# Kernel optimization log

Hardware: AMD Instinct MI355X
Metric: run time of the kernel (lower is better)

## Reference

```python
import jax, jax.numpy as jnp
import numpy as np

H = 4                      # num_heads hard-coded in SDHGNN
NAMES = ["self", "cross", "self", "cross"]
POOL_SIZES = [2, 2, 2, 2]
MIN_NGHS = 128             # minium_nghs
EPS = 1e-3                 # InstanceNorm1d eps


def _pw(x, W, b):
    # pointwise Conv1d(kernel=1): [B, Cin, N] -> [B, Cout, N]
    return jnp.einsum('oi,bin->bon', W, x) + b[None, :, None]


def _instnorm(x):
    # InstanceNorm1d (no affine): normalize over N per (B, C)
    m = jnp.mean(x, axis=2, keepdims=True)
    v = jnp.mean((x - m) ** 2, axis=2, keepdims=True)
    return (x - m) * jax.lax.rsqrt(v + EPS)


def _attn_prop(x, src, p):
    # SharedAttentionalPropagation (sharing_attention=False):
    # MultiHeadedAttention + concat + MLP residual update.
    Wq, bq, Wk, bk, Wv, bv, Wm, bm, W1, b1, W2, b2 = p
    B, D, N = x.shape
    dh = D // H
    q = _pw(x, Wq, bq).reshape(B, dh, H, N)
    k = _pw(src, Wk, bk).reshape(B, dh, H, -1)
    v = _pw(src, Wv, bv).reshape(B, dh, H, -1)
    scores = jnp.einsum('bdhn,bdhm->bhnm', q, k) * (dh ** -0.5)
    prob = jax.nn.softmax(scores, axis=-1)                     # [B,H,N,M]
    msg = jnp.einsum('bhnm,bdhm->bdhn', prob, v).reshape(B, D, N)
    msg = _pw(msg, Wm, bm)
    y = jnp.concatenate([x, msg], axis=1)                      # [B,2D,N]
    h = jax.nn.relu(_instnorm(_pw(y, W1, b1)))
    return x + _pw(h, W2, b2), prob


def _gather(x, idx):
    # x: [B,D,N], idx: [B,K] -> [B,D,K]
    return jnp.take_along_axis(
        x, jnp.broadcast_to(idx[:, None, :], (x.shape[0], x.shape[1], idx.shape[1])), axis=2)


def _pool(prob, idx, pool_size):
    # pooling_by_prob (4-D prob branch): mean over heads, sum over queries,
    # top-k by importance, sorted indices, gather global indexes.
    K = idx.shape[1]
    p = prob.mean(axis=1).sum(axis=1)                          # [B,K]
    k = min(max(K // pool_size, MIN_NGHS), K)
    _, top = jax.lax.top_k(p, k)
    top = jnp.sort(top, axis=1)
    return jnp.take_along_axis(idx, top, axis=1)


def setup_inputs() -> dict:
    key = jax.random.key(0)
    B, D, N, L = 2, 128, 2048, 4
    ks = jax.random.split(key, 16)
    s = lambda fan: 1.0 / np.sqrt(fan)
    inp = {
        'x0': jax.random.normal(ks[0], (B, D, N), jnp.float32),
        'x1': jax.random.normal(ks[1], (B, D, N), jnp.float32),
        'Wq': jax.random.normal(ks[2], (L, D, D), jnp.float32) * s(D),
        'bq': jax.random.normal(ks[3], (L, D), jnp.float32) * 0.01,
        'Wk': jax.random.normal(ks[4], (L, D, D), jnp.float32) * s(D),
        'bk': jax.random.normal(ks[5], (L, D), jnp.float32) * 0.01,
        'Wv': jax.random.normal(ks[6], (L, D, D), jnp.float32) * s(D),
        'bv': jax.random.normal(ks[7], (L, D), jnp.float32) * 0.01,
        'Wm': jax.random.normal(ks[8], (L, D, D), jnp.float32) * s(D),
        'bm': jax.random.normal(ks[9], (L, D), jnp.float32) * 0.01,
        'W1': jax.random.normal(ks[10], (L, 2 * D, 2 * D), jnp.float32) * s(2 * D),
        'b1': jax.random.normal(ks[11], (L, 2 * D), jnp.float32) * 0.01,
        'W2': jax.random.normal(ks[12], (L, D, 2 * D), jnp.float32) * s(2 * D),
        'b2': jnp.zeros((L, D), jnp.float32),  # nn.init.constant_(mlp[-1].bias, 0)
    }
    return inp


def reference(x0, x1, Wq, bq, Wk, bk, Wv, bv, Wm, bm, W1, b1, W2, b2):
    B, D, N = x0.shape
    idx0 = jnp.broadcast_to(jnp.arange(N, dtype=jnp.int32)[None], (B, N))
    idx1 = idx0
    for l, (name, ps) in enumerate(zip(NAMES, POOL_SIZES)):
        p = (Wq[l], bq[l], Wk[l], bk[l], Wv[l], bv[l],
             Wm[l], bm[l], W1[l], b1[l], W2[l], b2[l])
        if name == 'self':
            s0, s1 = _gather(x0, idx0), _gather(x1, idx1)
        else:
            s0, s1 = _gather(x1, idx1), _gather(x0, idx0)
        x0, prob0 = _attn_prop(x0, s0, p)
        x1, prob1 = _attn_prop(x1, s1, p)
        if name == 'self':
            idx0 = _pool(prob0, idx0, ps)
            idx1 = _pool(prob1, idx1, ps)
        else:
            idx1 = _pool(prob0, idx1, ps)
            idx0 = _pool(prob1, idx0, ps)
    return jnp.stack([x0, x1], axis=0)   # [2, B, D, N]
```

## Files before the change

kernel.cpp:

```cpp
#include <hip/hip_runtime.h>
#include <cstdint>
#include <cstddef>


#define NB 2
#define ND 128
#define NH 4
#define NN 2048
#define ND2 256
#define DN (ND*NN)
#define BDN (NB*DN)
#define QK_SCALE 0.2550348623f
#define IN_EPS 1e-3f

typedef unsigned short u16;
typedef __attribute__((ext_vector_type(8))) short short8;
typedef __attribute__((ext_vector_type(4))) float f32x4;

__device__ __forceinline__ u16 f2bf(float f) {
    unsigned u = __float_as_uint(f);
    return (u16)((u + 0x7fffu + ((u >> 16) & 1u)) >> 16);
}
__device__ __forceinline__ float bf2f(u16 h) {
    return __uint_as_float(((unsigned)h) << 16);
}
__device__ __forceinline__ float fexp2(float x) {
#if __has_builtin(__builtin_amdgcn_exp2f)
    return __builtin_amdgcn_exp2f(x);
#else
    return exp2f(x);
#endif
}
__device__ __forceinline__ unsigned cvtpk_bf16(float a, float b) {
    unsigned r;
    asm("v_cvt_pk_bf16_f32 %0, %1, %2" : "=v"(r) : "v"(a), "v"(b));
    return r;
}
#define ROR16F(x, N) __int_as_float(__builtin_amdgcn_update_dpp( \
    0, __float_as_int(x), 0x120 + (N), 0xF, 0xF, true))

__global__ __launch_bounds__(256) void init_kernel(
    const float* __restrict__ x0in, const float* __restrict__ x1in,
    float* __restrict__ out, int* __restrict__ idx0, int* __restrict__ idx1)
{
    int tid = blockIdx.x * 256 + threadIdx.x;
    const float4* a = (const float4*)x0in;
    const float4* b = (const float4*)x1in;
    float4* o = (float4*)out;
    o[tid] = a[tid];
    o[BDN/4 + tid] = b[tid];
    if (tid < NB*NN) {
        int v = tid & (NN-1);
        idx0[tid] = v;
        idx1[tid] = v;
    }
}

__global__ __launch_bounds__(256) void wrepack2_kernel(
    const float* __restrict__ Wq, const float* __restrict__ Wk,
    const float* __restrict__ Wv, const float* __restrict__ Wm,
    const float* __restrict__ W1, const float* __restrict__ W2,
    const float* __restrict__ bq, const float* __restrict__ bk,
    const float* __restrict__ bv, const float* __restrict__ bm,
    const float* __restrict__ b1,
    u16* __restrict__ whi, u16* __restrict__ wlo,
    float* __restrict__ bqp, float* __restrict__ bkp, float* __restrict__ bvp,
    float* __restrict__ b1p)
{
    int e = blockIdx.x * 256 + threadIdx.x;
    if (e < 655360) {
        int l = e / 163840, r = e - l*163840;
        float v;
        if (r < 49152) {
            int m = r >> 14;
            int rr = r & 16383;
            int o = rr >> 7, c = rr & 127;
            int so = (o & 31)*4 + (o >> 5);
            const float* W = (m == 0) ? Wq : ((m == 1) ? Wk : Wv);
            v = W[l*16384 + so*128 + c];
        } else if (r < 65536) {
            int rr = r - 49152;
            int o = rr >> 7, c = rr & 127;
            int sc = (c & 31)*4 + (c >> 5);
            v = Wm[l*16384 + o*128 + sc];
        } else if (r < 131072) {
            int rr = r - 65536;
            int c = rr & 255;
            if (c < 128) {
                v = W1[l*65536 + rr];
            } else {
                int o = rr >> 8, cc = c - 128;
                int sc = (cc & 31)*4 + (cc >> 5);
                const float* w1row = &W1[l*65536 + o*256 + 128];
                const float* wmcol = &Wm[l*16384 + sc];
                float acc = 0.f;
                #pragma unroll 4
                for (int k = 0; k < 128; ++k)
                    acc = fmaf(w1row[k], wmcol[k*128], acc);
                v = acc;
            }
        }
        else                   v = W2[l*32768 + r - 131072];
        u16 hb = f2bf(v);
        whi[e] = hb;
        wlo[e] = f2bf(v - bf2f(hb));
    } else if (e < 656896) {
        int eb = e - 655360;
        int l = eb / 384, rr = eb % 384;
        int which = rr >> 7, o = rr & 127;
        int so = (o & 31)*4 + (o >> 5);
        float v = (which == 0 ? bq : (which == 1 ? bk : bv))[l*128 + so];
        (which == 0 ? bqp : (which == 1 ? bkp : bvp))[l*128 + o] = v;
    } else if (e < 657920) {
        int idx = e - 656896;
        int l = idx >> 8, o = idx & 255;
        const float* w1row = &W1[l*65536 + o*256 + 128];
        const float* bmv = &bm[l*128];
        float acc = b1[l*256 + o];
        #pragma unroll 4
        for (int k = 0; k < 128; ++k)
            acc = fmaf(w1row[k], bmv[k], acc);
        b1p[l*256 + o] = acc;
    }
}

__global__ __launch_bounds__(256) void repack_xh_kernel(
    const float* __restrict__ in, u16* __restrict__ ohi, u16* __restrict__ olo)
{
    __shared__ float tile[32][68];
    int z = blockIdx.y >> 2, cg = blockIdx.y & 3;
    int n0 = blockIdx.x * 64;
    int t = threadIdx.x;
    {
        int i = t >> 3, nc = (t & 7) * 8;
        const float* src = &in[((size_t)z*128 + cg*32 + i)*NN + n0 + nc];
        float4 a = *(const float4*)src;
        float4 b = *(const float4*)(src + 4);
        tile[i][nc+0]=a.x; tile[i][nc+1]=a.y; tile[i][nc+2]=a.z; tile[i][nc+3]=a.w;
        tile[i][nc+4]=b.x; tile[i][nc+5]=b.y; tile[i][nc+6]=b.z; tile[i][nc+7]=b.w;
    }
    __syncthreads();
    int n = t >> 2, c8 = (t & 3) * 8;
    short8 hi, lo;
    #pragma unroll
    for (int j = 0; j < 8; ++j) {
        float v = tile[c8 + j][n];
        u16 h = f2bf(v);
        hi[j] = (short)h;
        lo[j] = (short)f2bf(v - bf2f(h));
    }
    size_t ob = ((size_t)z*NN + n0 + n)*128 + cg*32 + c8;
    *(short8*)&ohi[ob] = hi;
    *(short8*)&olo[ob] = lo;
}

__device__ __forceinline__ void gcore(
    u16* As0, u16* As1, u16* Bs0, u16* Bs1,
    const u16* __restrict__ Whi, const u16* __restrict__ Wlo, int o0, int Cin,
    const u16* __restrict__ B1hi, const u16* __restrict__ B1lo, int s1,
    const u16* __restrict__ B2hi, const u16* __restrict__ B2lo, int s2, int split,
    size_t brow, int n0, const int* __restrict__ idxp, int t, f32x4 acc[2][2])
{
    const int lane = t & 63, w = t >> 6;
    const int l15 = lane & 15, quad = lane >> 4;
    const int wr = (w & 1)*32, wc = (w >> 1)*32;
    const int ao = t >> 2, ak = (t & 3)*8;
    int grow = n0 + ao;
    if (idxp) grow = idxp[grow];

    short8 rA0, rA1, rB0, rB1;
    {
        size_t wa = (size_t)(o0 + ao)*Cin + ak;
        rA0 = *(const short8*)&Whi[wa];
        rA1 = *(const short8*)&Wlo[wa];
        int c = ak;
        const u16 *ph, *pl; size_t off;
        if (c < split) { ph = B1hi; pl = B1lo; off = (brow + grow)*s1 + c; }
        else { ph = B2hi; pl = B2lo; off = (brow + grow)*s2 + (c - split); }
        rB0 = *(const short8*)&ph[off];
        rB1 = *(const short8*)&pl[off];
    }
    for (int kc = 0; kc < Cin; kc += 32) {
        __syncthreads();
        *(short8*)&As0[ao*40 + ak] = rA0;
        *(short8*)&As1[ao*40 + ak] = rA1;
        *(short8*)&Bs0[ao*40 + ak] = rB0;
        *(short8*)&Bs1[ao*40 + ak] = rB1;
        if (kc + 32 < Cin) {
            size_t wa = (size_t)(o0 + ao)*Cin + kc + 32 + ak;
            rA0 = *(const short8*)&Whi[wa];
            rA1 = *(const short8*)&Wlo[wa];
            int c = kc + 32 + ak;
            const u16 *ph, *pl; size_t off;
            if (c < split) { ph = B1hi; pl = B1lo; off = (brow + grow)*s1 + c; }
            else { ph = B2hi; pl = B2lo; off = (brow + grow)*s2 + (c - split); }
            rB0 = *(const short8*)&ph[off];
            rB1 = *(const short8*)&pl[off];
        }
        __syncthreads();
        short8 Ah[2], Al[2], Bh[2], Bl[2];
        #pragma unroll
        for (int a = 0; a < 2; ++a) {
            Ah[a] = *(const short8*)&As0[(wr + a*16 + l15)*40 + quad*8];
            Al[a] = *(const short8*)&As1[(wr + a*16 + l15)*40 + quad*8];
        }
        #pragma unroll
        for (int c = 0; c < 2; ++c) {
            Bh[c] = *(const short8*)&Bs0[(wc + c*16 + l15)*40 + quad*8];
            Bl[c] = *(const short8*)&Bs1[(wc + c*16 + l15)*40 + quad*8];
        }
        #pragma unroll
        for (int a = 0; a < 2; ++a)
            #pragma unroll
            for (int c = 0; c < 2; ++c) {
                acc[a][c] = __builtin_amdgcn_mfma_f32_16x16x32_bf16(Ah[a], Bl[c], acc[a][c], 0,0,0);
                acc[a][c] = __builtin_amdgcn_mfma_f32_16x16x32_bf16(Al[a], Bh[c], acc[a][c], 0,0,0);
                acc[a][c] = __builtin_amdgcn_mfma_f32_16x16x32_bf16(Ah[a], Bh[c], acc[a][c], 0,0,0);
            }
    }
    __syncthreads();
}

__device__ __forceinline__ void gcore_w2(
    u16* As0, u16* As1, u16* Bs0, u16* Bs1,
    const u16* __restrict__ Whi, const u16* __restrict__ Wlo, int o0,
    const float* __restrict__ zft, const float* __restrict__ meanL,
    const float* __restrict__ ivL,
    size_t brow, int n0, int t, f32x4 acc[2][2])
{
    const int Cin = 256;
    const int lane = t & 63, w = t >> 6;
    const int l15 = lane & 15, quad = lane >> 4;
    const int wr = (w & 1)*32, wc = (w >> 1)*32;
    const int ao = t >> 2, ak = (t & 3)*8;
    const float* brows = &zft[(brow + n0 + ao)*256];

    short8 rA0, rA1, rBh, rBl;
    {
        size_t wa = (size_t)(o0 + ao)*Cin + ak;
        rA0 = *(const short8*)&Whi[wa];
        rA1 = *(const short8*)&Wlo[wa];
        float4 f0 = *(const float4*)&brows[ak];
        float4 f1 = *(const float4*)&brows[ak + 4];
        float f[8] = {f0.x,f0.y,f0.z,f0.w,f1.x,f1.y,f1.z,f1.w};
        #pragma unroll
        for (int j = 0; j < 8; ++j) {
            float v = (f[j] - meanL[ak + j]) * ivL[ak + j];
            v = v > 0.f ? v : 0.f;
            u16 hb = f2bf(v);
            rBh[j] = (short)hb;
            rBl[j] = (short)f2bf(v - bf2f(hb));
        }
    }
    for (int kc = 0; kc < Cin; kc += 32) {
        __syncthreads();
        *(short8*)&As0[ao*40 + ak] = rA0;
        *(short8*)&As1[ao*40 + ak] = rA1;
        *(short8*)&Bs0[ao*40 + ak] = rBh;
        *(short8*)&Bs1[ao*40 + ak] = rBl;
        float4 f0n, f1n;
        const bool more = (kc + 32 < Cin);
        if (more) {
            size_t wa = (size_t)(o0 + ao)*Cin + kc + 32 + ak;
            rA0 = *(const short8*)&Whi[wa];
            rA1 = *(const short8*)&Wlo[wa];
            f0n = *(const float4*)&brows[kc + 32 + ak];
            f1n = *(const float4*)&brows[kc + 32 + ak + 4];
        }
        __syncthreads();
        short8 Ah[2], Al[2], Bh[2], Bl[2];
        #pragma unroll
        for (int a = 0; a < 2; ++a) {
            Ah[a] = *(const short8*)&As0[(wr + a*16 + l15)*40 + quad*8];
            Al[a] = *(const short8*)&As1[(wr + a*16 + l15)*40 + quad*8];
        }
        #pragma unroll
        for (int c = 0; c < 2; ++c) {
            Bh[c] = *(const short8*)&Bs0[(wc + c*16 + l15)*40 + quad*8];
            Bl[c] = *(const short8*)&Bs1[(wc + c*16 + l15)*40 + quad*8];
        }
        #pragma unroll
        for (int a = 0; a < 2; ++a)
            #pragma unroll
            for (int c = 0; c < 2; ++c) {
                acc[a][c] = __builtin_amdgcn_mfma_f32_16x16x32_bf16(Ah[a], Bl[c], acc[a][c], 0,0,0);
                acc[a][c] = __builtin_amdgcn_mfma_f32_16x16x32_bf16(Al[a], Bh[c], acc[a][c], 0,0,0);
                acc[a][c] = __builtin_amdgcn_mfma_f32_16x16x32_bf16(Ah[a], Bh[c], acc[a][c], 0,0,0);
            }
        if (more) {
            float f[8] = {f0n.x,f0n.y,f0n.z,f0n.w,f1n.x,f1n.y,f1n.z,f1n.w};
            #pragma unroll
            for (int j = 0; j < 8; ++j) {
                int cc = kc + 32 + ak + j;
                float v = (f[j] - meanL[cc]) * ivL[cc];
                v = v > 0.f ? v : 0.f;
                u16 hb = f2bf(v);
                rBh[j] = (short)hb;
                rBl[j] = (short)f2bf(v - bf2f(hb));
            }
        }
    }
    __syncthreads();
}

__global__ __launch_bounds__(256) void qkv_kernel(
    const u16* __restrict__ Whi, const u16* __restrict__ Wlo,
    const float* __restrict__ bqp, const float* __restrict__ bkp,
    const float* __restrict__ bvp,
    const u16* __restrict__ xphi, const u16* __restrict__ xplo,
    const int* __restrict__ idx0, const int* __restrict__ idx1,
    int cross, int M,
    u16* __restrict__ qthi, u16* __restrict__ qtlo,
    u16* __restrict__ kthi, u16* __restrict__ ktlo,
    u16* __restrict__ vthi, float* __restrict__ p,
    float* __restrict__ gsum, float* __restrict__ gsq)
{
    __shared__ u16 gsm[10240];
    u16* As0 = gsm;  u16* As1 = gsm + 2560;
    u16* Bs0 = gsm + 5120; u16* Bs1 = gsm + 7680;
    float* tb = (float*)gsm;

    const int z = blockIdx.z;
    const int bx = blockIdx.x;
    const int t = threadIdx.x;
    const int lane = t & 63, w = t >> 6;
    const int l15 = lane & 15, quad = lane >> 4;
    const int wr = (w & 1)*32, wc = (w >> 1)*32;

    int role, o0, n0, nCols;
    const u16 *Wbh, *Wbl;
    const float* bias;
    if (bx < 64) {
        role = 0; o0 = (bx & 1)*64; n0 = (bx >> 1)*64; nCols = NN;
        Wbh = Whi; Wbl = Wlo; bias = bqp;
        if (t < 32) p[(size_t)z*NN + bx*32 + t] = 0.f;
        if (bx == 0) { gsum[z*256 + t] = 0.f; gsq[z*256 + t] = 0.f; }
    } else {
        int e = bx - 64;
        int kt = M >> 6;
        int ct = e % kt, rt = e / kt;
        n0 = ct*64; nCols = M;
        if (rt < 2) { role = 1; o0 = rt*64; Wbh = Whi+16384; Wbl = Wlo+16384; bias = bkp; }
        else        { role = 2; o0 = (rt-2)*64; Wbh = Whi+32768; Wbl = Wlo+32768; bias = bvp; }
    }
    size_t brow = (size_t)z * NN;
    const int* idxp = nullptr;
    if (role != 0) {
        int ss = cross ? 1 - (z >> 1) : (z >> 1);
        brow = (size_t)(ss*2 + (z & 1)) * NN;
        idxp = (ss ? idx1 : idx0) + (z & 1)*NN;
    }

    f32x4 acc[2][2];
    #pragma unroll
    for (int a = 0; a < 2; ++a)
        #pragma unroll
        for (int c = 0; c < 2; ++c) acc[a][c] = (f32x4){0.f,0.f,0.f,0.f};

    gcore(As0, As1, Bs0, Bs1, Wbh, Wbl, o0, 128,
          xphi, xplo, 128, xphi, xplo, 128, 128, brow, n0, idxp, t, acc);

    if (role == 2) {
        #pragma unroll
        for (int a = 0; a < 2; ++a)
            #pragma unroll
            for (int c = 0; c < 2; ++c)
                #pragma unroll
                for (int r = 0; r < 4; ++r) {
                    int row = o0 + wr + a*16 + quad*4 + r;
                    int m = n0 + wc + c*16 + l15;
                    float v = acc[a][c][r] + bias[row];
                    vthi[((size_t)(z*4 + (row>>5))*32 + (row&31))*(size_t)M + m] = f2bf(v);
                }
    } else {
        float scale = role ? 1.f : QK_SCALE;
        #pragma unroll
        for (int a = 0; a < 2; ++a)
            #pragma unroll
            for (int c = 0; c < 2; ++c)
                #pragma unroll
                for (int r = 0; r < 4; ++r) {
                    int rl = wr + a*16 + quad*4 + r;
                    tb[rl*66 + wc + c*16 + l15] = acc[a][c][r] + bias[o0 + rl];
                }
        __syncthreads();
        u16* ohi = role ? kthi : qthi;
        u16* olo = role ? ktlo : qtlo;
        int n = t >> 2, rb = (t & 3)*16;
        #pragma unroll
        for (int g = 0; g < 2; ++g) {
            short8 hi, lo;
            #pragma unroll
            for (int j = 0; j < 8; ++j) {
                float v = tb[(rb + g*8 + j)*66 + n] * scale;
                u16 hb = f2bf(v);
                hi[j] = (short)hb;
                lo[j] = (short)f2bf(v - bf2f(hb));
            }
            int rowg = o0 + rb + g*8;
            size_t ob = ((size_t)(z*4 + (rowg >> 5))*nCols + n0 + n)*32 + (rowg & 31);
            *(short8*)&ohi[ob] = hi;
            *(short8*)&olo[ob] = lo;
        }
    }
}

__global__ __launch_bounds__(512, 4) void attn4_kernel(
    const u16* __restrict__ qthi, const u16* __restrict__ qtlo,
    const u16* __restrict__ kthi, const u16* __restrict__ ktlo,
    const u16* __restrict__ vthi, int M,
    u16* __restrict__ msghi, u16* __restrict__ msglo, float* __restrict__ p)
{
    __shared__ float pcolA[2048], pcolB[2048];
    __shared__ float obuf[96*66];
    __shared__ float redm[4][64], redl[4][64];
    __shared__ float rowM[64], rowIV[64];

    const int t = threadIdx.x;
    const int lane = t & 63, wave = t >> 6;
    const int l15 = lane & 15, quad = lane >> 4;
    const int qp = wave & 1, mh = wave >> 1;
    const int h = blockIdx.y, z = blockIdx.z;
    const int zh = z*4 + h;
    const int n0 = blockIdx.x * 64;

    for (int i = t; i < M; i += 512) { pcolA[i] = 0.f; pcolB[i] = 0.f; }

    short8 qBh[2], qBl[2];
    #pragma unroll
    for (int qt = 0; qt < 2; ++qt) {
        size_t qb = ((size_t)zh*NN + n0 + qp*32 + qt*16 + l15)*32 + quad*8;
        qBh[qt] = *(const short8*)&qthi[qb];
        qBl[qt] = *(const short8*)&qtlo[qb];
    }

    const int nch = M >> 7;
    const size_t kb0 = ((size_t)zh*M + mh*32 + l15)*32 + quad*8;
    const u16* kbh = kthi + kb0;
    const u16* kbl = ktlo + kb0;
    const u16* vb = vthi + ((size_t)zh*32 + l15)*M + mh*32 + quad*8;

    float rm[2] = {-1e30f, -1e30f}, rl[2] = {0.f, 0.f};

    for (int ch = 0; ch < nch; ++ch) {
        const int co = ch*128*32;
        #pragma unroll
        for (int mt = 0; mt < 2; ++mt) {
            short8 kh = *(const short8*)&kbh[co + mt*512];
            short8 kl = *(const short8*)&kbl[co + mt*512];
            __builtin_amdgcn_s_setprio(1);
            f32x4 av[2];
            #pragma unroll
            for (int qt = 0; qt < 2; ++qt) {
                f32x4 a = {0.f,0.f,0.f,0.f};
                a = __builtin_amdgcn_mfma_f32_16x16x32_bf16(kh, qBl[qt], a, 0,0,0);
                a = __builtin_amdgcn_mfma_f32_16x16x32_bf16(kl, qBh[qt], a, 0,0,0);
                a = __builtin_amdgcn_mfma_f32_16x16x32_bf16(kh, qBh[qt], a, 0,0,0);
                av[qt] = a;
            }
            __builtin_amdgcn_s_setprio(0);
            #pragma unroll
            for (int qt = 0; qt < 2; ++qt) {
                f32x4 a = av[qt];
                float bm = fmaxf(fmaxf(a[0],a[1]), fmaxf(a[2],a[3]));
                float bs = fexp2(a[0]-bm)+fexp2(a[1]-bm)+fexp2(a[2]-bm)+fexp2(a[3]-bm);
                if (bm > rm[qt]) { rl[qt] = rl[qt]*fexp2(rm[qt]-bm) + bs; rm[qt] = bm; }
                else rl[qt] += bs*fexp2(bm - rm[qt]);
            }
        }
    }

    #pragma unroll
    for (int qt = 0; qt < 2; ++qt) {
        #pragma unroll
        for (int off = 16; off <= 32; off <<= 1) {
            float om = __shfl_xor(rm[qt], off);
            float ol = __shfl_xor(rl[qt], off);
            float nm = fmaxf(rm[qt], om);
            rl[qt] = rl[qt]*fexp2(rm[qt]-nm) + ol*fexp2(om-nm);
            rm[qt] = nm;
        }
        if (quad == 0) {
            redm[mh][qp*32 + qt*16 + l15] = rm[qt];
            redl[mh][qp*32 + qt*16 + l15] = rl[qt];
        }
    }
    __syncthreads();
    if (t < 64) {
        float m = redm[0][t], l = redl[0][t];
        #pragma unroll
        for (int w2 = 1; w2 < 4; ++w2) {
            float om = redm[w2][t];
            float nm = fmaxf(m, om);
            l = l*fexp2(m - nm) + redl[w2][t]*fexp2(om - nm);
            m = nm;
        }
        rowM[t] = m;
        rowIV[t] = 1.f / l;
    }
    __syncthreads();
    float myRM[2], myRIV[2];
    #pragma unroll
    for (int qt = 0; qt < 2; ++qt) {
        myRM[qt]  = rowM[qp*32 + qt*16 + l15];
        myRIV[qt] = rowIV[qp*32 + qt*16 + l15];
    }

    f32x4 oa[2][2];
    #pragma unroll
    for (int qt = 0; qt < 2; ++qt)
        #pragma unroll
        for (int dt = 0; dt < 2; ++dt) oa[qt][dt] = (f32x4){0.f,0.f,0.f,0.f};

    const int aA = (l15 + 32*(quad & 1))*4;
    const int aB = aA + 64;
    const bool mtsel = (quad >= 2);
    float* pcolQ = qp ? pcolB : pcolA;

    for (int ch = 0; ch < nch; ++ch) {
        const int m0 = ch << 7;
        const int co = ch*128*32;

        float pr[2][2][4];
        #pragma unroll
        for (int mt = 0; mt < 2; ++mt) {
            short8 kh = *(const short8*)&kbh[co + mt*512];
            short8 kl = *(const short8*)&kbl[co + mt*512];
            __builtin_amdgcn_s_setprio(1);
            f32x4 av[2];
            #pragma unroll
            for (int qt = 0; qt < 2; ++qt) {
                f32x4 a = {0.f,0.f,0.f,0.f};
                a = __builtin_amdgcn_mfma_f32_16x16x32_bf16(kh, qBl[qt], a, 0,0,0);
                a = __builtin_amdgcn_mfma_f32_16x16x32_bf16(kl, qBh[qt], a, 0,0,0);
                a = __builtin_amdgcn_mfma_f32_16x16x32_bf16(kh, qBh[qt], a, 0,0,0);
                av[qt] = a;
            }
            __builtin_amdgcn_s_setprio(0);
            #pragma unroll
            for (int qt = 0; qt < 2; ++qt)
                #pragma unroll
                for (int r = 0; r < 4; ++r)
                    pr[qt][mt][r] = fexp2(av[qt][r] - myRM[qt]);
        }

        #pragma unroll
        for (int mt = 0; mt < 2; ++mt)
            #pragma unroll
            for (int r = 0; r < 4; ++r) {
                float ps = pr[0][mt][r]*myRIV[0] + pr[1][mt][r]*myRIV[1];
                ps += ROR16F(ps, 8);
                ps += ROR16F(ps, 4);
                ps += ROR16F(ps, 2);
                ps += ROR16F(ps, 1);
                if (l15 == 0)
                    pcolQ[m0 + mh*32 + mt*16 + quad*4 + r] = ps;
            }

        short8 vA[2];
        #pragma unroll
        for (int dt = 0; dt < 2; ++dt)
            vA[dt] = *(const short8*)&vb[(size_t)dt*16*M + m0];

        #pragma unroll
        for (int qt = 0; qt < 2; ++qt) {
            unsigned pk00 = cvtpk_bf16(pr[qt][0][0], pr[qt][0][1]);
            unsigned pk01 = cvtpk_bf16(pr[qt][0][2], pr[qt][0][3]);
            unsigned pk10 = cvtpk_bf16(pr[qt][1][0], pr[qt][1][1]);
            unsigned pk11 = cvtpk_bf16(pr[qt][1][2], pr[qt][1][3]);
            unsigned a0 = (unsigned)__builtin_amdgcn_ds_bpermute(aA, (int)pk00);
            unsigned a1 = (unsigned)__builtin_amdgcn_ds_bpermute(aA, (int)pk01);
            unsigned a2 = (unsigned)__builtin_amdgcn_ds_bpermute(aA, (int)pk10);
            unsigned a3 = (unsigned)__builtin_amdgcn_ds_bpermute(aA, (int)pk11);
            unsigned b0 = (unsigned)__builtin_amdgcn_ds_bpermute(aB, (int)pk00);
            unsigned b1 = (unsigned)__builtin_amdgcn_ds_bpermute(aB, (int)pk01);
            unsigned b2 = (unsigned)__builtin_amdgcn_ds_bpermute(aB, (int)pk10);
            unsigned b3 = (unsigned)__builtin_amdgcn_ds_bpermute(aB, (int)pk11);
            union { unsigned u[4]; short8 s; } fb;
            fb.u[0] = mtsel ? a2 : a0;
            fb.u[1] = mtsel ? a3 : a1;
            fb.u[2] = mtsel ? b2 : b0;
            fb.u[3] = mtsel ? b3 : b1;
            __builtin_amdgcn_s_setprio(1);
            #pragma unroll
            for (int dt = 0; dt < 2; ++dt)
                oa[qt][dt] = __builtin_amdgcn_mfma_f32_16x16x32_bf16(vA[dt], fb.s, oa[qt][dt], 0,0,0);
            __builtin_amdgcn_s_setprio(0);
        }
    }

    if (mh > 0) {
        #pragma unroll
        for (int qt = 0; qt < 2; ++qt)
            #pragma unroll
            for (int dt = 0; dt < 2; ++dt)
                #pragma unroll
                for (int r = 0; r < 4; ++r) {
                    int q = qp*32 + qt*16 + l15;
                    int d = dt*16 + quad*4 + r;
                    obuf[((mh-1)*32 + d)*66 + q] = oa[qt][dt][r];
                }
    }
    __syncthreads();
    if (mh == 0) {
        #pragma unroll
        for (int qt = 0; qt < 2; ++qt)
            #pragma unroll
            for (int dt = 0; dt < 2; ++dt)
                #pragma unroll
                for (int r = 0; r < 4; ++r) {
                    int q = qp*32 + qt*16 + l15;
                    int d = dt*16 + quad*4 + r;
                    float v = oa[qt][dt][r];
                    #pragma unroll
                    for (int w2 = 0; w2 < 3; ++w2)
                        v += obuf[(w2*32 + d)*66 + q];
                    obuf[d*66 + q] = v * myRIV[qt];
                }
    }
    __syncthreads();
    {
        int tt = t & 255;
        int n = tt >> 2, i8 = (tt & 3)*8;
        short8 o8;
        if (t < 256) {
            #pragma unroll
            for (int j = 0; j < 8; ++j) o8[j] = (short)f2bf(obuf[(i8+j)*66 + n]);
            *(short8*)&msghi[((size_t)z*NN + n0 + n)*128 + h*32 + i8] = o8;
        } else {
            #pragma unroll
            for (int j = 0; j < 8; ++j) {
                float v = obuf[(i8+j)*66 + n];
                u16 hb = f2bf(v);
                o8[j] = (short)f2bf(v - bf2f(hb));
            }
            *(short8*)&msglo[((size_t)z*NN + n0 + n)*128 + h*32 + i8] = o8;
        }
    }
    for (int i = t; i < M; i += 512)
        atomicAdd(&p[(size_t)z*NN + i], (pcolA[i] + pcolB[i])*0.25f);
}

__global__ __launch_bounds__(256) void w1_kernel(
    const u16* __restrict__ W1h, const u16* __restrict__ W1l,
    const float* __restrict__ b1,
    const u16* __restrict__ xphi, const u16* __restrict__ xplo,
    const u16* __restrict__ m2hi, const u16* __restrict__ m2lo,
    float* __restrict__ zft, float* __restrict__ gsum, float* __restrict__ gsq)
{
    __shared__ u16 gsm[10240];
    u16* As0 = gsm;  u16* As1 = gsm + 2560;
    u16* Bs0 = gsm + 5120; u16* Bs1 = gsm + 7680;
    float* tb = (float*)gsm;

    const int z = blockIdx.z, o0 = blockIdx.y*64, n0 = blockIdx.x*64;
    const int t = threadIdx.x;
    const int lane = t & 63, w = t >> 6;
    const int l15 = lane & 15, quad = lane >> 4;
    const int wr = (w & 1)*32, wc = (w >> 1)*32;

    f32x4 acc[2][2];
    #pragma unroll
    for (int a = 0; a < 2; ++a)
        #pragma unroll
        for (int c = 0; c < 2; ++c) acc[a][c] = (f32x4){0.f,0.f,0.f,0.f};
    gcore(As0, As1, Bs0, Bs1, W1h, W1l, o0, 256,
          xphi, xplo, 128, m2hi, m2lo, 128, 128,
          (size_t)z*NN, n0, nullptr, t, acc);

    float ssum[2][4], ssq[2][4];
    #pragma unroll
    for (int a = 0; a < 2; ++a)
        #pragma unroll
        for (int r = 0; r < 4; ++r) { ssum[a][r] = 0.f; ssq[a][r] = 0.f; }
    #pragma unroll
    for (int a = 0; a < 2; ++a)
        #pragma unroll
        for (int c = 0; c < 2; ++c)
            #pragma unroll
            for (int r = 0; r < 4; ++r) {
                int rl = wr + a*16 + quad*4 + r;
                int cl = wc + c*16 + l15;
                float v = acc[a][c][r] + b1[o0 + rl];
                tb[rl*66 + cl] = v;
                ssum[a][r] += v;
                ssq[a][r] = fmaf(v, v, ssq[a][r]);
            }
    #pragma unroll
    for (int a = 0; a < 2; ++a)
        #pragma unroll
        for (int r = 0; r < 4; ++r) {
            float s = ssum[a][r], q2 = ssq[a][r];
            #pragma unroll
            for (int o = 1; o < 16; o <<= 1) {
                s  += __shfl_xor(s, o);
                q2 += __shfl_xor(q2, o);
            }
            if (l15 == 0) {
                int row = o0 + wr + a*16 + quad*4 + r;
                atomicAdd(&gsum[z*256 + row], s);
                atomicAdd(&gsq[z*256 + row], q2);
            }
        }
    __syncthreads();
    int n = t >> 2, rb = (t & 3)*16;
    #pragma unroll
    for (int g = 0; g < 2; ++g) {
        float4 v0, v1;
        v0.x = tb[(rb + g*8 + 0)*66 + n];
        v0.y = tb[(rb + g*8 + 1)*66 + n];
        v0.z = tb[(rb + g*8 + 2)*66 + n];
        v0.w = tb[(rb + g*8 + 3)*66 + n];
        v1.x = tb[(rb + g*8 + 4)*66 + n];
        v1.y = tb[(rb + g*8 + 5)*66 + n];
        v1.z = tb[(rb + g*8 + 6)*66 + n];
        v1.w = tb[(rb + g*8 + 7)*66 + n];
        float* dst = &zft[((size_t)z*NN + n0 + n)*256 + o0 + rb + g*8];
        *(float4*)dst = v0;
        *(float4*)(dst + 4) = v1;
    }
}

__global__ __launch_bounds__(256) void w2_kernel(
    const u16* __restrict__ W2h, const u16* __restrict__ W2l,
    const float* __restrict__ b2,
    const float* __restrict__ zft, const float* __restrict__ gsum,
    const float* __restrict__ gsq,
    float* __restrict__ out, u16* __restrict__ xphi, u16* __restrict__ xplo,
    int writeplanes)
{
    __shared__ u16 gsm[10240];
    __shared__ float meanL[256], ivL[256];
    u16* As0 = gsm;  u16* As1 = gsm + 2560;
    u16* Bs0 = gsm + 5120; u16* Bs1 = gsm + 7680;
    float* tb = (float*)gsm;

    const int z = blockIdx.z, o0 = blockIdx.y*64, n0 = blockIdx.x*64;
    const int t = threadIdx.x;
    const int lane = t & 63, w = t >> 6;
    const int l15 = lane & 15, quad = lane >> 4;
    const int wr = (w & 1)*32, wc = (w >> 1)*32;

    {
        float mean = gsum[z*256 + t] * (1.f/NN);
        float var  = gsq[z*256 + t] * (1.f/NN) - mean*mean;
        meanL[t] = mean;
        ivL[t] = rsqrtf(var + IN_EPS);
    }
    __syncthreads();

    f32x4 acc[2][2];
    #pragma unroll
    for (int a = 0; a < 2; ++a)
        #pragma unroll
        for (int c = 0; c < 2; ++c) acc[a][c] = (f32x4){0.f,0.f,0.f,0.f};
    gcore_w2(As0, As1, Bs0, Bs1, W2h, W2l, o0,
             zft, meanL, ivL, (size_t)z*NN, n0, t, acc);

    #pragma unroll
    for (int a = 0; a < 2; ++a)
        #pragma unroll
        for (int c = 0; c < 2; ++c)
            #pragma unroll
            for (int r = 0; r < 4; ++r) {
                int rl = wr + a*16 + quad*4 + r;
                int rowg = o0 + rl;
                int n = n0 + wc + c*16 + l15;
                size_t oi = ((size_t)z*128 + rowg)*NN + n;
                float v = acc[a][c][r] + b2[rowg] + out[oi];
                out[oi] = v;
                tb[rl*66 + wc + c*16 + l15] = v;
            }
    __syncthreads();
    if (writeplanes) {
        int n = t >> 2, rb = (t & 3)*16;
        #pragma unroll
        for (int g = 0; g < 2; ++g) {
            short8 hi, lo;
            #pragma unroll
            for (int j = 0; j < 8; ++j) {
                float v = tb[(rb + g*8 + j)*66 + n];
                u16 hb = f2bf(v);
                hi[j] = (short)hb;
                lo[j] = (short)f2bf(v - bf2f(hb));
            }
            size_t ob = ((size_t)z*NN + n0 + n)*128 + o0 + rb + g*8;
            *(short8*)&xphi[ob] = hi;
            *(short8*)&xplo[ob] = lo;
        }
    }
}

__global__ __launch_bounds__(256) void rank_kernel(
    const float* __restrict__ p, int* __restrict__ rank, int M)
{
    int zz = blockIdx.y;
    __shared__ float pv[2048];
    for (int i = threadIdx.x; i < M; i += 256) pv[i] = p[(size_t)zz*NN + i];
    __syncthreads();
    int i = blockIdx.x * 256 + threadIdx.x;
    if (i < M) {
        float pi = pv[i];
        int r = 0;
        for (int j = 0; j < M; ++j) {
            float pj = pv[j];
            r += (pj > pi) ? 1 : ((pj == pi && j < i) ? 1 : 0);
        }
        rank[zz*NN + i] = r;
    }
}

__global__ __launch_bounds__(256) void select_kernel(
    const int* __restrict__ rank, int* __restrict__ idx0, int* __restrict__ idx1,
    int M, int k, int cross)
{
    int z = blockIdx.x;
    int st = z >> 1, b = z & 1;
    int ts = cross ? 1 - st : st;
    int* idx = (ts ? idx1 : idx0) + b * NN;
    const int* rk = rank + z * NN;
    __shared__ int sel[2048], idv[2048], sa[2048], sb[2048];
    int t = threadIdx.x;
    for (int i = t; i < M; i += 256) {
        int s = rk[i] < k ? 1 : 0;
        sel[i] = s;
        sa[i] = s;
        idv[i] = idx[i];
    }
    __syncthreads();
    int* src = sa; int* dst = sb;
    for (int off = 1; off < M; off <<= 1) {
        for (int i = t; i < M; i += 256)
            dst[i] = src[i] + (i >= off ? src[i - off] : 0);
        __syncthreads();
        int* tmp = src; src = dst; dst = tmp;
    }
    for (int i = t; i < M; i += 256)
        if (sel[i]) idx[src[i] - 1] = idv[i];
}

extern "C" void kernel_launch(void* const* d_in, const int* in_sizes, int n_in,
                              void* d_out, int out_size, void* d_ws, size_t ws_size,
                              hipStream_t stream)
{
    const float* x0in = (const float*)d_in[0];
    const float* x1in = (const float*)d_in[1];
    const float* Wq = (const float*)d_in[2];
    const float* bq = (const float*)d_in[3];
    const float* Wk = (const float*)d_in[4];
    const float* bk = (const float*)d_in[5];
    const float* Wv = (const float*)d_in[6];
    const float* bv = (const float*)d_in[7];
    const float* Wm = (const float*)d_in[8];
    const float* bm = (const float*)d_in[9];
    const float* W1 = (const float*)d_in[10];
    const float* b1 = (const float*)d_in[11];
    const float* W2 = (const float*)d_in[12];
    const float* b2 = (const float*)d_in[13];

    float* out = (float*)d_out;
    float* ws  = (float*)d_ws;

    const size_t U = 1048576;
    u16* ub   = (u16*)ws;
    u16* xphi = ub;            u16* xplo = ub + U;
    u16* qthi = ub + 2*U;      u16* qtlo = ub + 3*U;
    u16* kthi = ub + 4*U;      u16* ktlo = ub + 5*U;
    u16* vthi = ub + 6*U;
    u16* msghi = ub + 7*U;     u16* msglo = ub + 8*U;
    u16* whi  = ub + 15*U;     u16* wlo = whi + 655360;
    float* zft = (float*)(ub + 2*U);
    float* ft = (float*)(wlo + 655360);
    float* bqp = ft;           float* bkp = ft + 512;      float* bvp = ft + 1024;
    float* gsum = ft + 1536;   float* gsq = ft + 2560;
    float* p = ft + 3584;
    int* idx0 = (int*)(p + 4*NN);
    int* idx1 = idx0 + NB*NN;
    int* rankb = idx1 + NB*NN;
    float* b1p = (float*)(rankb + 4*NN);

    init_kernel<<<BDN/4/256, 256, 0, stream>>>(x0in, x1in, out, idx0, idx1);
    wrepack2_kernel<<<2570, 256, 0, stream>>>(Wq, Wk, Wv, Wm, W1, W2, bq, bk, bv,
                                              bm, b1, whi, wlo, bqp, bkp, bvp, b1p);
    repack_xh_kernel<<<dim3(32, 16), 256, 0, stream>>>(out, xphi, xplo);

    const int Ms[4] = {2048, 1024, 512, 256};
    for (int l = 0; l < 4; ++l) {
        int M = Ms[l];
        int k_new = (M/2 < 128) ? 128 : M/2;
        int cross = l & 1;
        size_t lw = (size_t)l * 163840;
        const u16* Wlh = whi + lw;  const u16* Wll = wlo + lw;

        qkv_kernel<<<dim3(64 + 4*(M/64), 1, 4), 256, 0, stream>>>(
            Wlh, Wll, bqp + l*128, bkp + l*128, bvp + l*128,
            xphi, xplo, idx0, idx1, cross, M,
            qthi, qtlo, kthi, ktlo, vthi, p, gsum, gsq);

        attn4_kernel<<<dim3(32, NH, 4), 512, 0, stream>>>(
            qthi, qtlo, kthi, ktlo, vthi, M, msghi, msglo, p);

        w1_kernel<<<dim3(32, 4, 4), 256, 0, stream>>>(
            Wlh + 65536, Wll + 65536, b1p + l*256,
            xphi, xplo, msghi, msglo, zft, gsum, gsq);

        w2_kernel<<<dim3(32, 2, 4), 256, 0, stream>>>(
            Wlh + 131072, Wll + 131072, b2 + l*128,
            zft, gsum, gsq, out, xphi, xplo, (l < 3) ? 1 : 0);

        rank_kernel<<<dim3((M+255)/256, 4), 256, 0, stream>>>(p, rankb, M);
        select_kernel<<<4, 256, 0, stream>>>(rankb, idx0, idx1, M, k_new, cross);
    }
}
```

Before: 506.3 us.

## Halve attention query tile, split prob accumulator per head, stagger atomics

The attention kernel now processes 32 queries per block instead of 64, doubling the grid to 64x4x4 and raising the launch-bounds occupancy hint to 8 blocks. The column-probability accumulator is split into a per-head buffer, each block's atomic adds start at a block-dependent offset, and rank_kernel sums the four head slices. The aim is more parallelism and less atomic contention on the shared probability array. In exchange, each block recomputes the full K pass for fewer queries, so K/V loads and the two-pass softmax overhead per query roughly double.

```diff
diff --git a/kernel.cpp b/kernel.cpp
--- a/kernel.cpp
+++ b/kernel.cpp
@@ -312,7 +312,7 @@
     int cross, int M,
     u16* __restrict__ qthi, u16* __restrict__ qtlo,
     u16* __restrict__ kthi, u16* __restrict__ ktlo,
-    u16* __restrict__ vthi, float* __restrict__ p,
+    u16* __restrict__ vthi, float* __restrict__ p4,
     float* __restrict__ gsum, float* __restrict__ gsq)
 {
     __shared__ u16 gsm[10240];
@@ -333,7 +333,8 @@
     if (bx < 64) {
         role = 0; o0 = (bx & 1)*64; n0 = (bx >> 1)*64; nCols = NN;
         Wbh = Whi; Wbl = Wlo; bias = bqp;
-        if (t < 32) p[(size_t)z*NN + bx*32 + t] = 0.f;
+        if (t < 128)
+            p4[((size_t)(z*4 + (t >> 5)))*NN + bx*32 + (t & 31)] = 0.f;
         if (bx == 0) { gsum[z*256 + t] = 0.f; gsq[z*256 + t] = 0.f; }
     } else {
         int e = bx - 64;
@@ -405,33 +406,32 @@
     }
 }
 
-__global__ __launch_bounds__(512, 4) void attn4_kernel(
+__global__ __launch_bounds__(512, 8) void attn4_kernel(
     const u16* __restrict__ qthi, const u16* __restrict__ qtlo,
     const u16* __restrict__ kthi, const u16* __restrict__ ktlo,
     const u16* __restrict__ vthi, int M,
-    u16* __restrict__ msghi, u16* __restrict__ msglo, float* __restrict__ p)
+    u16* __restrict__ msghi, u16* __restrict__ msglo, float* __restrict__ p4)
 {
     __shared__ float pcolA[2048], pcolB[2048];
-    __shared__ float obuf[96*66];
-    __shared__ float redm[4][64], redl[4][64];
-    __shared__ float rowM[64], rowIV[64];
+    __shared__ float obuf[96*34];
+    __shared__ float redm[4][32], redl[4][32];
+    __shared__ float rowM[32], rowIV[32];
 
     const int t = threadIdx.x;
     const int lane = t & 63, wave = t >> 6;
     const int l15 = lane & 15, quad = lane >> 4;
-    const int qp = wave & 1, mh = wave >> 1;
+    const int qh = wave & 1, mh = wave >> 1;
     const int h = blockIdx.y, z = blockIdx.z;
     const int zh = z*4 + h;
-    const int n0 = blockIdx.x * 64;
+    const int n0 = blockIdx.x * 32;
 
     for (int i = t; i < M; i += 512) { pcolA[i] = 0.f; pcolB[i] = 0.f; }
 
-    short8 qBh[2], qBl[2];
-    #pragma unroll
-    for (int qt = 0; qt < 2; ++qt) {
-        size_t qb = ((size_t)zh*NN + n0 + qp*32 + qt*16 + l15)*32 + quad*8;
-        qBh[qt] = *(const short8*)&qthi[qb];
-        qBl[qt] = *(const short8*)&qtlo[qb];
+    short8 qBh, qBl;
+    {
+        size_t qb = ((size_t)zh*NN + n0 + qh*16 + l15)*32 + quad*8;
+        qBh = *(const short8*)&qthi[qb];
+        qBl = *(const short8*)&qtlo[qb];
     }
 
     const int nch = M >> 7;
@@ -440,53 +440,43 @@
     const u16* kbl = ktlo + kb0;
     const u16* vb = vthi + ((size_t)zh*32 + l15)*M + mh*32 + quad*8;
 
-    float rm[2] = {-1e30f, -1e30f}, rl[2] = {0.f, 0.f};
+    float rm = -1e30f, rl = 0.f;
 
     for (int ch = 0; ch < nch; ++ch) {
-        const int co = ch*128*32;
+        const int co = ch*4096;
         #pragma unroll
         for (int mt = 0; mt < 2; ++mt) {
             short8 kh = *(const short8*)&kbh[co + mt*512];
             short8 kl = *(const short8*)&kbl[co + mt*512];
             __builtin_amdgcn_s_setprio(1);
-            f32x4 av[2];
-            #pragma unroll
-            for (int qt = 0; qt < 2; ++qt) {
-                f32x4 a = {0.f,0.f,0.f,0.f};
-                a = __builtin_amdgcn_mfma_f32_16x16x32_bf16(kh, qBl[qt], a, 0,0,0);
-                a = __builtin_amdgcn_mfma_f32_16x16x32_bf16(kl, qBh[qt], a, 0,0,0);
-                a = __builtin_amdgcn_mfma_f32_16x16x32_bf16(kh, qBh[qt], a, 0,0,0);
-                av[qt] = a;
-            }
+            f32x4 a = {0.f,0.f,0.f,0.f};
+            a = __builtin_amdgcn_mfma_f32_16x16x32_bf16(kh, qBl, a, 0,0,0);
+            a = __builtin_amdgcn_mfma_f32_16x16x32_bf16(kl, qBh, a, 0,0,0);
+            a = __builtin_amdgcn_mfma_f32_16x16x32_bf16(kh, qBh, a, 0,0,0);
             __builtin_amdgcn_s_setprio(0);
-            #pragma unroll
-            for (int qt = 0; qt < 2; ++qt) {
-                f32x4 a = av[qt];
-                float bm = fmaxf(fmaxf(a[0],a[1]), fmaxf(a[2],a[3]));
-                float bs = fexp2(a[0]-bm)+fexp2(a[1]-bm)+fexp2(a[2]-bm)+fexp2(a[3]-bm);
-                if (bm > rm[qt]) { rl[qt] = rl[qt]*fexp2(rm[qt]-bm) + bs; rm[qt] = bm; }
-                else rl[qt] += bs*fexp2(bm - rm[qt]);
-            }
-        }
-    }
-
-    #pragma unroll
-    for (int qt = 0; qt < 2; ++qt) {
+            float bm = fmaxf(fmaxf(a[0],a[1]), fmaxf(a[2],a[3]));
+            float bs = fexp2(a[0]-bm)+fexp2(a[1]-bm)+fexp2(a[2]-bm)+fexp2(a[3]-bm);
+            if (bm > rm) { rl = rl*fexp2(rm-bm) + bs; rm = bm; }
+            else rl += bs*fexp2(bm - rm);
+        }
+    }
+
+    {
         #pragma unroll
         for (int off = 16; off <= 32; off <<= 1) {
-            float om = __shfl_xor(rm[qt], off);
-            float ol = __shfl_xor(rl[qt], off);
-            float nm = fmaxf(rm[qt], om);
-            rl[qt] = rl[qt]*fexp2(rm[qt]-nm) + ol*fexp2(om-nm);
-            rm[qt] = nm;
+            float om = __shfl_xor(rm, off);
+            float ol = __shfl_xor(rl, off);
+            float nm = fmaxf(rm, om);
+            rl = rl*fexp2(rm-nm) + ol*fexp2(om-nm);
+            rm = nm;
         }
         if (quad == 0) {
-            redm[mh][qp*32 + qt*16 + l15] = rm[qt];
-            redl[mh][qp*32 + qt*16 + l15] = rl[qt];
-        }
-    }
-    __syncthreads();
-    if (t < 64) {
+            redm[mh][qh*16 + l15] = rm;
+            redl[mh][qh*16 + l15] = rl;
+        }
+    }
+    __syncthreads();
+    if (t < 32) {
         float m = redm[0][t], l = redl[0][t];
         #pragma unroll
         for (int w2 = 1; w2 < 4; ++w2) {
@@ -499,56 +489,43 @@
         rowIV[t] = 1.f / l;
     }
     __syncthreads();
-    float myRM[2], myRIV[2];
-    #pragma unroll
-    for (int qt = 0; qt < 2; ++qt) {
-        myRM[qt]  = rowM[qp*32 + qt*16 + l15];
-        myRIV[qt] = rowIV[qp*32 + qt*16 + l15];
-    }
-
-    f32x4 oa[2][2];
-    #pragma unroll
-    for (int qt = 0; qt < 2; ++qt)
-        #pragma unroll
-        for (int dt = 0; dt < 2; ++dt) oa[qt][dt] = (f32x4){0.f,0.f,0.f,0.f};
+    float myRM  = rowM[qh*16 + l15];
+    float myRIV = rowIV[qh*16 + l15];
+
+    f32x4 oa[2];
+    #pragma unroll
+    for (int dt = 0; dt < 2; ++dt) oa[dt] = (f32x4){0.f,0.f,0.f,0.f};
 
     const int aA = (l15 + 32*(quad & 1))*4;
     const int aB = aA + 64;
     const bool mtsel = (quad >= 2);
-    float* pcolQ = qp ? pcolB : pcolA;
+    float* pcolQ = qh ? pcolB : pcolA;
 
     for (int ch = 0; ch < nch; ++ch) {
         const int m0 = ch << 7;
-        const int co = ch*128*32;
-
-        float pr[2][2][4];
+        const int co = ch*4096;
+
+        float pr[2][4];
         #pragma unroll
         for (int mt = 0; mt < 2; ++mt) {
             short8 kh = *(const short8*)&kbh[co + mt*512];
             short8 kl = *(const short8*)&kbl[co + mt*512];
             __builtin_amdgcn_s_setprio(1);
-            f32x4 av[2];
-            #pragma unroll
-            for (int qt = 0; qt < 2; ++qt) {
-                f32x4 a = {0.f,0.f,0.f,0.f};
-                a = __builtin_amdgcn_mfma_f32_16x16x32_bf16(kh, qBl[qt], a, 0,0,0);
-                a = __builtin_amdgcn_mfma_f32_16x16x32_bf16(kl, qBh[qt], a, 0,0,0);
-                a = __builtin_amdgcn_mfma_f32_16x16x32_bf16(kh, qBh[qt], a, 0,0,0);
-                av[qt] = a;
-            }
+            f32x4 a = {0.f,0.f,0.f,0.f};
+            a = __builtin_amdgcn_mfma_f32_16x16x32_bf16(kh, qBl, a, 0,0,0);
+            a = __builtin_amdgcn_mfma_f32_16x16x32_bf16(kl, qBh, a, 0,0,0);
+            a = __builtin_amdgcn_mfma_f32_16x16x32_bf16(kh, qBh, a, 0,0,0);
             __builtin_amdgcn_s_setprio(0);
             #pragma unroll
-            for (int qt = 0; qt < 2; ++qt)
-                #pragma unroll
-                for (int r = 0; r < 4; ++r)
-                    pr[qt][mt][r] = fexp2(av[qt][r] - myRM[qt]);
+            for (int r = 0; r < 4; ++r)
+                pr[mt][r] = fexp2(a[r] - myRM);
         }
 
         #pragma unroll
         for (int mt = 0; mt < 2; ++mt)
             #pragma unroll
             for (int r = 0; r < 4; ++r) {
-                float ps = pr[0][mt][r]*myRIV[0] + pr[1][mt][r]*myRIV[1];
+                float ps = pr[mt][r]*myRIV;
                 ps += ROR16F(ps, 8);
                 ps += ROR16F(ps, 4);
                 ps += ROR16F(ps, 2);
@@ -562,12 +539,11 @@
         for (int dt = 0; dt < 2; ++dt)
             vA[dt] = *(const short8*)&vb[(size_t)dt*16*M + m0];
 
-        #pragma unroll
-        for (int qt = 0; qt < 2; ++qt) {
-            unsigned pk00 = cvtpk_bf16(pr[qt][0][0], pr[qt][0][1]);
-            unsigned pk01 = cvtpk_bf16(pr[qt][0][2], pr[qt][0][3]);
-            unsigned pk10 = cvtpk_bf16(pr[qt][1][0], pr[qt][1][1]);
-            unsigned pk11 = cvtpk_bf16(pr[qt][1][2], pr[qt][1][3]);
+        {
+            unsigned pk00 = cvtpk_bf16(pr[0][0], pr[0][1]);
+            unsigned pk01 = cvtpk_bf16(pr[0][2], pr[0][3]);
+            unsigned pk10 = cvtpk_bf16(pr[1][0], pr[1][1]);
+            unsigned pk11 = cvtpk_bf16(pr[1][2], pr[1][3]);
             unsigned a0 = (unsigned)__builtin_amdgcn_ds_bpermute(aA, (int)pk00);
             unsigned a1 = (unsigned)__builtin_amdgcn_ds_bpermute(aA, (int)pk01);
             unsigned a2 = (unsigned)__builtin_amdgcn_ds_bpermute(aA, (int)pk10);
@@ -584,61 +560,63 @@
             __builtin_amdgcn_s_setprio(1);
             #pragma unroll
             for (int dt = 0; dt < 2; ++dt)
-                oa[qt][dt] = __builtin_amdgcn_mfma_f32_16x16x32_bf16(vA[dt], fb.s, oa[qt][dt], 0,0,0);
+                oa[dt] = __builtin_amdgcn_mfma_f32_16x16x32_bf16(vA[dt], fb.s, oa[dt], 0,0,0);
             __builtin_amdgcn_s_setprio(0);
         }
     }
 
     if (mh > 0) {
         #pragma unroll
-        for (int qt = 0; qt < 2; ++qt)
-            #pragma unroll
-            for (int dt = 0; dt < 2; ++dt)
+        for (int dt = 0; dt < 2; ++dt)
+            #pragma unroll
+            for (int r = 0; r < 4; ++r) {
+                int q = qh*16 + l15;
+                int d = dt*16 + quad*4 + r;
+                obuf[((mh-1)*32 + d)*34 + q] = oa[dt][r];
+            }
+    }
+    __syncthreads();
+    if (mh == 0) {
+        #pragma unroll
+        for (int dt = 0; dt < 2; ++dt)
+            #pragma unroll
+            for (int r = 0; r < 4; ++r) {
+                int q = qh*16 + l15;
+                int d = dt*16 + quad*4 + r;
+                float v = oa[dt][r];
                 #pragma unroll
-                for (int r = 0; r < 4; ++r) {
-                    int q = qp*32 + qt*16 + l15;
-                    int d = dt*16 + quad*4 + r;
-                    obuf[((mh-1)*32 + d)*66 + q] = oa[qt][dt][r];
-                }
-    }
-    __syncthreads();
-    if (mh == 0) {
-        #pragma unroll
-        for (int qt = 0; qt < 2; ++qt)
-            #pragma unroll
-            for (int dt = 0; dt < 2; ++dt)
-                #pragma unroll
-                for (int r = 0; r < 4; ++r) {
-                    int q = qp*32 + qt*16 + l15;
-                    int d = dt*16 + quad*4 + r;
-                    float v = oa[qt][dt][r];
-                    #pragma unroll
-                    for (int w2 = 0; w2 < 3; ++w2)
-                        v += obuf[(w2*32 + d)*66 + q];
-                    obuf[d*66 + q] = v * myRIV[qt];
-                }
-    }
-    __syncthreads();
-    {
-        int tt = t & 255;
+                for (int w2 = 0; w2 < 3; ++w2)
+                    v += obuf[(w2*32 + d)*34 + q];
+                obuf[d*34 + q] = v * myRIV;
+            }
+    }
+    __syncthreads();
+    if (t < 256) {
+        int which = t >> 7;
+        int tt = t & 127;
         int n = tt >> 2, i8 = (tt & 3)*8;
         short8 o8;
-        if (t < 256) {
-            #pragma unroll
-            for (int j = 0; j < 8; ++j) o8[j] = (short)f2bf(obuf[(i8+j)*66 + n]);
+        if (which == 0) {
+            #pragma unroll
+            for (int j = 0; j < 8; ++j) o8[j] = (short)f2bf(obuf[(i8+j)*34 + n]);
             *(short8*)&msghi[((size_t)z*NN + n0 + n)*128 + h*32 + i8] = o8;
         } else {
             #pragma unroll
             for (int j = 0; j < 8; ++j) {
-                float v = obuf[(i8+j)*66 + n];
+                float v = obuf[(i8+j)*34 + n];
                 u16 hb = f2bf(v);
                 o8[j] = (short)f2bf(v - bf2f(hb));
             }
             *(short8*)&msglo[((size_t)z*NN + n0 + n)*128 + h*32 + i8] = o8;
         }
     }
-    for (int i = t; i < M; i += 512)
-        atomicAdd(&p[(size_t)z*NN + i], (pcolA[i] + pcolB[i])*0.25f);
+    {
+        int sh = (blockIdx.x * 32) & (M - 1);
+        for (int i = t; i < M; i += 512) {
+            int ii = (i + sh) & (M - 1);
+            atomicAdd(&p4[(size_t)zh*NN + ii], (pcolA[ii] + pcolB[ii])*0.25f);
+        }
+    }
 }
 
 __global__ __launch_bounds__(256) void w1_kernel(
@@ -792,11 +770,14 @@
 }
 
 __global__ __launch_bounds__(256) void rank_kernel(
-    const float* __restrict__ p, int* __restrict__ rank, int M)
+    const float* __restrict__ p4, int* __restrict__ rank, int M)
 {
     int zz = blockIdx.y;
     __shared__ float pv[2048];
-    for (int i = threadIdx.x; i < M; i += 256) pv[i] = p[(size_t)zz*NN + i];
+    for (int i = threadIdx.x; i < M; i += 256) {
+        size_t b = (size_t)zz*4*NN + i;
+        pv[i] = p4[b] + p4[b + NN] + p4[b + 2*NN] + p4[b + 3*NN];
+    }
     __syncthreads();
     int i = blockIdx.x * 256 + threadIdx.x;
     if (i < M) {
@@ -868,13 +849,13 @@
     u16* kthi = ub + 4*U;      u16* ktlo = ub + 5*U;
     u16* vthi = ub + 6*U;
     u16* msghi = ub + 7*U;     u16* msglo = ub + 8*U;
+    float* p4 = (float*)(ub + 9*U);
     u16* whi  = ub + 15*U;     u16* wlo = whi + 655360;
     float* zft = (float*)(ub + 2*U);
     float* ft = (float*)(wlo + 655360);
     float* bqp = ft;           float* bkp = ft + 512;      float* bvp = ft + 1024;
     float* gsum = ft + 1536;   float* gsq = ft + 2560;
-    float* p = ft + 3584;
-    int* idx0 = (int*)(p + 4*NN);
+    int* idx0 = (int*)(ft + 3584 + 4*NN);
     int* idx1 = idx0 + NB*NN;
     int* rankb = idx1 + NB*NN;
     float* b1p = (float*)(rankb + 4*NN);
@@ -895,10 +876,10 @@
         qkv_kernel<<<dim3(64 + 4*(M/64), 1, 4), 256, 0, stream>>>(
             Wlh, Wll, bqp + l*128, bkp + l*128, bvp + l*128,
             xphi, xplo, idx0, idx1, cross, M,
-            qthi, qtlo, kthi, ktlo, vthi, p, gsum, gsq);
-
-        attn4_kernel<<<dim3(32, NH, 4), 512, 0, stream>>>(
-            qthi, qtlo, kthi, ktlo, vthi, M, msghi, msglo, p);
+            qthi, qtlo, kthi, ktlo, vthi, p4, gsum, gsq);
+
+        attn4_kernel<<<dim3(64, NH, 4), 512, 0, stream>>>(
+            qthi, qtlo, kthi, ktlo, vthi, M, msghi, msglo, p4);
 
         w1_kernel<<<dim3(32, 4, 4), 256, 0, stream>>>(
             Wlh + 65536, Wll + 65536, b1p + l*256,
@@ -908,7 +889,7 @@
             Wlh + 131072, Wll + 131072, b2 + l*128,
             zft, gsum, gsq, out, xphi, xplo, (l < 3) ? 1 : 0);
 
-        rank_kernel<<<dim3((M+255)/256, 4), 256, 0, stream>>>(p, rankb, M);
+        rank_kernel<<<dim3((M+255)/256, 4), 256, 0, stream>>>(p4, rankb, M);
         select_kernel<<<4, 256, 0, stream>>>(rankb, idx0, idx1, M, k_new, cross);
     }
 }
```

After: 571.9 us. 1.13x slower.
